# Kernel optimization log

Hardware: AMD Instinct MI355X
Metric: run time of the kernel (lower is better)

The kernel has to match this reference:

```python
import jax, jax.numpy as jnp
import numpy as np

NUM_HEADS = 16
HEAD_DIM = 64
DIM = NUM_HEADS * HEAD_DIM
ROPE_BASE = 10000.0
EPS = 1e-6


def rotate_half(x):
    # pairs (x0,x1) -> (-x1, x0), interleaved on last dim
    x_even = x[..., ::2]
    x_odd = x[..., 1::2]
    return jnp.stack((-x_odd, x_even), axis=-1).reshape(x.shape)


def apply_rope(q, k, positions, base=ROPE_BASE):
    d = q.shape[-1]
    inv_freq = 1.0 / (base ** (jnp.arange(0, d, 2, dtype=jnp.float32) / d))
    angles = positions.astype(jnp.float32)[..., None] * inv_freq  # [B, L, d/2]
    cos = jnp.repeat(jnp.cos(angles), 2, axis=-1).astype(q.dtype)[:, None, :, :]  # [B,1,L,d]
    sin = jnp.repeat(jnp.sin(angles), 2, axis=-1).astype(q.dtype)[:, None, :, :]
    return q * cos + rotate_half(q) * sin, k * cos + rotate_half(k) * sin


def per_head_layernorm(x, weight):
    # x: [B, H, L, d]; weight: [H, d]; bias is zeros (qkv_bias=False)
    mu = jnp.mean(x, axis=-1, keepdims=True)
    var = jnp.mean(jnp.square(x - mu), axis=-1, keepdims=True)
    xn = (x - mu) * jax.lax.rsqrt(var + EPS)
    return xn * weight[None, :, None, :]


def setup_inputs() -> dict:
    key = jax.random.key(0)
    k1, k2, k3, k4, k5 = jax.random.split(key, 5)
    B, L = 2, 2048
    x = jax.random.normal(k1, (B, L, DIM), dtype=jnp.float32)
    mask = jnp.ones((B, L, L), dtype=bool)
    positions = jnp.broadcast_to(jnp.arange(L, dtype=jnp.int64 if jax.config.jax_enable_x64 else jnp.int32), (B, L))
    s = 1.0 / np.sqrt(DIM)
    W_qkv = jax.random.normal(k2, (DIM, 3 * DIM), dtype=jnp.float32) * s
    W_out = jax.random.normal(k3, (DIM, DIM), dtype=jnp.float32) * s
    qn_w = jnp.ones((NUM_HEADS, HEAD_DIM), dtype=jnp.float32)
    kn_w = jnp.ones((NUM_HEADS, HEAD_DIM), dtype=jnp.float32)
    return {"x": x, "mask": mask, "positions": positions,
            "W_qkv": W_qkv, "W_out": W_out, "qn_w": qn_w, "kn_w": kn_w}


def reference(x, mask, positions, W_qkv, W_out, qn_w, kn_w):
    B, L, D = x.shape
    scale = HEAD_DIM ** -0.5
    qkv = x @ W_qkv  # [B, L, 3D]
    qkv = qkv.reshape(B, L, 3, NUM_HEADS, HEAD_DIM)
    qkv = jnp.transpose(qkv, (2, 0, 3, 1, 4))  # [3, B, H, L, d]
    q, k, v = qkv[0], qkv[1], qkv[2]
    q = per_head_layernorm(q, qn_w)
    k = per_head_layernorm(k, kn_w)
    q, k = apply_rope(q, k, positions)
    attn = jnp.einsum('bhqd,bhkd->bhqk', q, k) * scale  # [B, H, L, L]
    attn = jnp.where(mask[:, None, :, :], attn, -jnp.inf)
    attn = jax.nn.softmax(attn, axis=-1)
    out = jnp.einsum('bhqk,bhkd->bhqd', attn, v)  # [B, H, L, d]
    out = jnp.transpose(out, (0, 2, 1, 3)).reshape(B, L, D)
    return out @ W_out
```

## Files before the change

### kernel.cpp

```cpp
#include <hip/hip_runtime.h>


typedef __bf16 bf16x8 __attribute__((ext_vector_type(8)));
typedef __bf16 bf16x2 __attribute__((ext_vector_type(2)));
typedef float f32x4 __attribute__((ext_vector_type(4)));

#define QSCALE 0.1803368802f

__device__ __forceinline__ float bf2f(unsigned short u) {
  unsigned int v = ((unsigned int)u) << 16;
  float f;
  __builtin_memcpy(&f, &v, 4);
  return f;
}
__device__ __forceinline__ unsigned short f2bf(float f) {
  unsigned int v;
  __builtin_memcpy(&v, &f, 4);
  v += 0x7fffu + ((v >> 16) & 1u);
  return (unsigned short)(v >> 16);
}
__device__ __forceinline__ unsigned short f2bf_hw(float f) {
  __bf16 h = (__bf16)f;
  unsigned short u;
  __builtin_memcpy(&u, &h, 2);
  return u;
}
__device__ __forceinline__ unsigned int pack2(float a, float b) {
  bf16x2 t;
  t[0] = (__bf16)a;
  t[1] = (__bf16)b;
  unsigned int u;
  __builtin_memcpy(&u, &t, 4);
  return u;
}
__device__ __forceinline__ void gl_lds16(const unsigned short* g, unsigned short* l) {
  __builtin_amdgcn_global_load_lds(
      (const __attribute__((address_space(1))) unsigned int*)g,
      (__attribute__((address_space(3))) unsigned int*)l, 16, 0, 0);
}

__global__ __launch_bounds__(256) void prep(
    const float* __restrict__ x, const float* __restrict__ W_qkv,
    const float* __restrict__ W_out, const int* __restrict__ positions,
    unsigned short* __restrict__ xb,
    unsigned short* __restrict__ Wt_qkv, unsigned short* __restrict__ Wt_out,
    float2* __restrict__ lut) {
  __shared__ float tile[64][65];
  const int bid = blockIdx.x, t = threadIdx.x;
  if (bid < 4096) {
    int i = (bid * 256 + t) * 4;
    float4 v = *reinterpret_cast<const float4*>(x + i);
    ushort4 o;
    o.x = f2bf(v.x); o.y = f2bf(v.y); o.z = f2bf(v.z); o.w = f2bf(v.w);
    *reinterpret_cast<ushort4*>(xb + i) = o;
    return;
  }
  if (bid >= 5120) {
    int idx = (bid - 5120) * 256 + t;
    int m = idx >> 5, p = idx & 31;
    float pos = (float)positions[m];
    float invf = __builtin_amdgcn_exp2f(-(float)(2 * p) * (13.2877124f / 64.0f));
    float rev = pos * invf * 0.15915494f;
    rev -= floorf(rev);
    lut[idx] = make_float2(__builtin_amdgcn_cosf(rev), __builtin_amdgcn_sinf(rev));
    return;
  }
  const float* W; unsigned short* Wt; int Nd, bn, bk;
  if (bid < 4864) {
    int id = bid - 4096; W = W_qkv; Wt = Wt_qkv; Nd = 3072; bn = id % 48; bk = id / 48;
  } else {
    int id = bid - 4864; W = W_out; Wt = Wt_out; Nd = 1024; bn = id % 16; bk = id / 16;
  }
  const int Kd = 1024;
#pragma unroll
  for (int i = 0; i < 16; i++) {
    int idx = i * 256 + t;
    int k = idx >> 6, n = idx & 63;
    tile[k][n] = W[(size_t)(bk * 64 + k) * Nd + bn * 64 + n];
  }
  __syncthreads();
#pragma unroll
  for (int i = 0; i < 16; i++) {
    int idx = i * 256 + t;
    int n = idx >> 6, k = idx & 63;
    Wt[(size_t)(bn * 64 + n) * Kd + bk * 64 + k] = f2bf(tile[k][n]);
  }
}

__global__ __launch_bounds__(256, 3) void gemm_qkv(
    const unsigned short* __restrict__ A,
    const unsigned short* __restrict__ Bt,
    const float* __restrict__ qn_w, const float* __restrict__ kn_w,
    const float2* __restrict__ lut,
    unsigned short* __restrict__ Qr,
    unsigned short* __restrict__ Kr,
    unsigned short* __restrict__ Vt, int K) {
  __shared__ __align__(16) unsigned short As[2][128 * 32];
  __shared__ __align__(16) unsigned short Bs[2][128 * 32];
  const int tid = threadIdx.x;
  const int lane = tid & 63, wid = tid >> 6;
  const int quad = lane >> 4, l16 = lane & 15;
  const int wr = wid >> 1, wc = wid & 1;
  const int bn = blockIdx.x, bm = blockIdx.y;
  const unsigned short* Ab = A + (size_t)bm * 128 * K;
  const unsigned short* Bb = Bt + (size_t)bn * 128 * K;

  f32x4 acc[4][4] = {};

  const int c0 = tid, c1 = tid + 256;
  const int ar0 = c0 >> 2, ag0 = ((c0 & 3) ^ ((ar0 >> 1) & 3)) * 8;
  const int ar1 = c1 >> 2, ag1 = ((c1 & 3) ^ ((ar1 >> 1) & 3)) * 8;

  gl_lds16(Ab + (size_t)ar0 * K + ag0, &As[0][c0 * 8]);
  gl_lds16(Ab + (size_t)ar1 * K + ag1, &As[0][c1 * 8]);
  gl_lds16(Bb + (size_t)ar0 * K + ag0, &Bs[0][c0 * 8]);
  gl_lds16(Bb + (size_t)ar1 * K + ag1, &Bs[0][c1 * 8]);

  const int iters = K >> 5;
  for (int it = 0; it < iters; it++) {
    const int cur = it & 1;
    __builtin_amdgcn_s_barrier();
    if (it + 1 < iters) {
      const int k0 = (it + 1) << 5, nb = cur ^ 1;
      gl_lds16(Ab + (size_t)ar0 * K + k0 + ag0, &As[nb][c0 * 8]);
      gl_lds16(Ab + (size_t)ar1 * K + k0 + ag1, &As[nb][c1 * 8]);
      gl_lds16(Bb + (size_t)ar0 * K + k0 + ag0, &Bs[nb][c0 * 8]);
      gl_lds16(Bb + (size_t)ar1 * K + k0 + ag1, &Bs[nb][c1 * 8]);
      __builtin_amdgcn_sched_barrier(0);
      asm volatile("s_waitcnt vmcnt(4)" ::: "memory");
    } else {
      __builtin_amdgcn_sched_barrier(0);
      asm volatile("s_waitcnt vmcnt(0)" ::: "memory");
    }
    __builtin_amdgcn_sched_barrier(0);
    __builtin_amdgcn_s_setprio(1);
    const unsigned short* Ac = As[cur];
    const unsigned short* Bc = Bs[cur];
    bf16x8 af[4], bfr[4];
#pragma unroll
    for (int i = 0; i < 4; i++) {
      int m = wr * 64 + i * 16 + l16;
      af[i] = *reinterpret_cast<const bf16x8*>(&Ac[m * 32 + ((quad ^ ((m >> 1) & 3)) * 8)]);
    }
#pragma unroll
    for (int j = 0; j < 4; j++) {
      int n = wc * 64 + j * 16 + l16;
      bfr[j] = *reinterpret_cast<const bf16x8*>(&Bc[n * 32 + ((quad ^ ((n >> 1) & 3)) * 8)]);
    }
#pragma unroll
    for (int i = 0; i < 4; i++)
#pragma unroll
      for (int j = 0; j < 4; j++)
        acc[i][j] = __builtin_amdgcn_mfma_f32_16x16x32_bf16(af[i], bfr[j], acc[i][j], 0, 0, 0);
    __builtin_amdgcn_s_setprio(0);
  }

  const int sec = bn >> 3;
  const int h = (bn & 7) * 2 + wc;
  const int b = bm >> 4;
  if (sec < 2) {
    const float* gw = sec ? kn_w : qn_w;
    unsigned short* dst = sec ? Kr : Qr;
    const float oscale = sec ? 1.0f : QSCALE;
    float w4[4];
#pragma unroll
    for (int j = 0; j < 4; j++) w4[j] = gw[h * 64 + j * 16 + l16];
#pragma unroll
    for (int i = 0; i < 4; i++)
#pragma unroll
      for (int r = 0; r < 4; r++) {
        int m = bm * 128 + wr * 64 + i * 16 + quad * 4 + r;
        int l = m & 2047;
        const float2* lrow = lut + m * 32;
        float2 cs4[4];
#pragma unroll
        for (int j = 0; j < 4; j++) cs4[j] = lrow[j * 8 + (l16 >> 1)];
        float sum = acc[i][0][r] + acc[i][1][r] + acc[i][2][r] + acc[i][3][r];
        float sq = acc[i][0][r] * acc[i][0][r] + acc[i][1][r] * acc[i][1][r] +
                   acc[i][2][r] * acc[i][2][r] + acc[i][3][r] * acc[i][3][r];
#pragma unroll
        for (int off = 1; off < 16; off <<= 1) {
          sum += __shfl_xor(sum, off);
          sq += __shfl_xor(sq, off);
        }
        float mu = sum * (1.0f / 64.0f);
        float var = sq * (1.0f / 64.0f) - mu * mu;
        float rs = rsqrtf(fmaxf(var, 0.0f) + 1e-6f);
#pragma unroll
        for (int j = 0; j < 4; j++) {
          float y = (acc[i][j][r] - mu) * rs * w4[j];
          float p = __shfl_xor(y, 1);
          float o = (l16 & 1) ? (y * cs4[j].x + p * cs4[j].y)
                              : (y * cs4[j].x - p * cs4[j].y);
          dst[((size_t)(b * 16 + h) * 2048 + l) * 64 + j * 16 + l16] = f2bf(o * oscale);
        }
      }
  } else {
#pragma unroll
    for (int i = 0; i < 4; i++) {
      int lp = (bm * 128 + wr * 64 + (i >> 1) * 32 + quad * 8 + (i & 1) * 4) & 2047;
#pragma unroll
      for (int j = 0; j < 4; j++) {
        int d = j * 16 + l16;
        uint2 v;
        v.x = pack2(acc[i][j][0], acc[i][j][1]);
        v.y = pack2(acc[i][j][2], acc[i][j][3]);
        *reinterpret_cast<uint2*>(&Vt[((size_t)(b * 16 + h) * 64 + d) * 2048 + lp]) = v;
      }
    }
  }
}

__global__ __launch_bounds__(512, 4) void attn_kernel(
    const unsigned short* __restrict__ Q,
    const unsigned short* __restrict__ K,
    const unsigned short* __restrict__ Vt,
    unsigned short* __restrict__ O) {
  __shared__ __align__(16) unsigned short Ks[2][2][64 * 64];
  __shared__ __align__(16) unsigned short Vs[2][2][64 * 64];

  int bid = blockIdx.x;
  int id = (bid & 7) * 64 + (bid >> 3);
  const int qt = id & 15; id >>= 4;
  const int h = id & 15;  const int b = id >> 4;
  const int tid = threadIdx.x;
  const int lane = tid & 63, wid = tid >> 6;
  const int half = wid >> 2, wg = wid & 3;
  const int quad = lane >> 4, l16 = lane & 15;

  const unsigned short* Qb = Q + (size_t)(b * 16 + h) * 2048 * 64;
  const unsigned short* Kb = K + (size_t)(b * 16 + h) * 2048 * 64;
  const unsigned short* Vb = Vt + (size_t)(b * 16 + h) * 64 * 2048;

  const int qbase = qt * 128 + wg * 32;
  bf16x8 qf[2][2];
#pragma unroll
  for (int g = 0; g < 2; g++)
#pragma unroll
    for (int d = 0; d < 2; d++)
      qf[g][d] = *reinterpret_cast<const bf16x8*>(
          &Qb[(size_t)(qbase + g * 16 + l16) * 64 + d * 32 + quad * 8]);

  bf16x8 ones8;
#pragma unroll
  for (int i = 0; i < 8; i++) ones8[i] = (__bf16)1.0f;

  f32x4 o[2][4] = {};
  f32x4 lacc[2] = {};

  const int ltid = tid & 255;
  const int c0 = ltid, c1 = ltid + 256;
  const int r0 = c0 >> 3, g0 = ((c0 & 7) ^ (r0 & 7)) * 8;
  const int r1 = c1 >> 3, g1 = ((c1 & 7) ^ (r1 & 7)) * 8;
  const int kb0 = half * 1024;

  gl_lds16(&Kb[(size_t)(kb0 + r0) * 64 + g0], &Ks[half][0][c0 * 8]);
  gl_lds16(&Kb[(size_t)(kb0 + r1) * 64 + g1], &Ks[half][0][c1 * 8]);
  gl_lds16(&Vb[(size_t)r0 * 2048 + kb0 + g0], &Vs[half][0][c0 * 8]);
  gl_lds16(&Vb[(size_t)r1 * 2048 + kb0 + g1], &Vs[half][0][c1 * 8]);

  for (int kt = 0; kt < 16; kt++) {
    const int cur = kt & 1;
    __builtin_amdgcn_s_barrier();
    if (kt + 1 < 16) {
      const int ko = kb0 + (kt + 1) * 64, nb = cur ^ 1;
      gl_lds16(&Kb[(size_t)(ko + r0) * 64 + g0], &Ks[half][nb][c0 * 8]);
      gl_lds16(&Kb[(size_t)(ko + r1) * 64 + g1], &Ks[half][nb][c1 * 8]);
      gl_lds16(&Vb[(size_t)r0 * 2048 + ko + g0], &Vs[half][nb][c0 * 8]);
      gl_lds16(&Vb[(size_t)r1 * 2048 + ko + g1], &Vs[half][nb][c1 * 8]);
      __builtin_amdgcn_sched_barrier(0);
      asm volatile("s_waitcnt vmcnt(4)" ::: "memory");
    } else {
      __builtin_amdgcn_sched_barrier(0);
      asm volatile("s_waitcnt vmcnt(0)" ::: "memory");
    }
    __builtin_amdgcn_sched_barrier(0);
    const unsigned short* Kc = Ks[half][cur];
    const unsigned short* Vc = Vs[half][cur];

    __builtin_amdgcn_s_setprio(1);
    f32x4 s4a[4] = {}, s4b[4] = {};
#pragma unroll
    for (int kg = 0; kg < 4; kg++) {
      int row = kg * 16 + l16;
      bf16x8 kf0 = *reinterpret_cast<const bf16x8*>(
          &Kc[row * 64 + ((quad ^ (row & 7)) * 8)]);
      bf16x8 kf1 = *reinterpret_cast<const bf16x8*>(
          &Kc[row * 64 + (((4 + quad) ^ (row & 7)) * 8)]);
      s4a[kg] = __builtin_amdgcn_mfma_f32_16x16x32_bf16(kf0, qf[0][0], s4a[kg], 0, 0, 0);
      s4a[kg] = __builtin_amdgcn_mfma_f32_16x16x32_bf16(kf1, qf[0][1], s4a[kg], 0, 0, 0);
      s4b[kg] = __builtin_amdgcn_mfma_f32_16x16x32_bf16(kf0, qf[1][0], s4b[kg], 0, 0, 0);
      s4b[kg] = __builtin_amdgcn_mfma_f32_16x16x32_bf16(kf1, qf[1][1], s4b[kg], 0, 0, 0);
    }
    float pva[4][4], pvb[4][4];
#pragma unroll
    for (int kg = 0; kg < 4; kg++)
#pragma unroll
      for (int r = 0; r < 4; r++) {
        pva[kg][r] = __builtin_amdgcn_exp2f(s4a[kg][r]);
        pvb[kg][r] = __builtin_amdgcn_exp2f(s4b[kg][r]);
      }
    union u32x4v { unsigned int u[4]; bf16x8 v; };
    u32x4v paa[2], pab[2];
#pragma unroll
    for (int c = 0; c < 2; c++) {
      paa[c].u[0] = pack2(pva[c * 2][0], pva[c * 2][1]);
      paa[c].u[1] = pack2(pva[c * 2][2], pva[c * 2][3]);
      paa[c].u[2] = pack2(pva[c * 2 + 1][0], pva[c * 2 + 1][1]);
      paa[c].u[3] = pack2(pva[c * 2 + 1][2], pva[c * 2 + 1][3]);
      pab[c].u[0] = pack2(pvb[c * 2][0], pvb[c * 2][1]);
      pab[c].u[1] = pack2(pvb[c * 2][2], pvb[c * 2][3]);
      pab[c].u[2] = pack2(pvb[c * 2 + 1][0], pvb[c * 2 + 1][1]);
      pab[c].u[3] = pack2(pvb[c * 2 + 1][2], pvb[c * 2 + 1][3]);
    }
#pragma unroll
    for (int c = 0; c < 2; c++) {
      lacc[0] = __builtin_amdgcn_mfma_f32_16x16x32_bf16(paa[c].v, ones8, lacc[0], 0, 0, 0);
      lacc[1] = __builtin_amdgcn_mfma_f32_16x16x32_bf16(pab[c].v, ones8, lacc[1], 0, 0, 0);
#pragma unroll
      for (int i = 0; i < 4; i++) {
        int row = i * 16 + l16;
        bf16x8 vfr = *reinterpret_cast<const bf16x8*>(
            &Vc[row * 64 + (((c * 4 + quad) ^ (row & 7)) * 8)]);
        o[0][i] = __builtin_amdgcn_mfma_f32_16x16x32_bf16(paa[c].v, vfr, o[0][i], 0, 0, 0);
        o[1][i] = __builtin_amdgcn_mfma_f32_16x16x32_bf16(pab[c].v, vfr, o[1][i], 0, 0, 0);
      }
    }
    __builtin_amdgcn_s_setprio(0);
  }

  __syncthreads();
  float* Om = (float*)&Ks[0][0][0];
  float* Lm = (float*)&Vs[0][0][0];
  if (half == 0) {
#pragma unroll
    for (int g = 0; g < 2; g++) {
#pragma unroll
      for (int i = 0; i < 4; i++)
#pragma unroll
        for (int r = 0; r < 4; r++)
          Om[(wg * 32 + g * 16 + quad * 4 + r) * 64 + i * 16 + l16] = o[g][i][r];
      if (l16 == 0) {
#pragma unroll
        for (int r = 0; r < 4; r++)
          Lm[wg * 32 + g * 16 + quad * 4 + r] = lacc[g][r];
      }
    }
  }
  __syncthreads();
  if (half == 1) {
#pragma unroll
    for (int g = 0; g < 2; g++) {
#pragma unroll
      for (int r = 0; r < 4; r++) {
        float lt = lacc[g][r] + Lm[wg * 32 + g * 16 + quad * 4 + r];
        float inv = 1.0f / lt;
        int q = qbase + g * 16 + quad * 4 + r;
#pragma unroll
        for (int i = 0; i < 4; i++) {
          float sum = o[g][i][r] + Om[(wg * 32 + g * 16 + quad * 4 + r) * 64 + i * 16 + l16];
          O[((size_t)(b * 2048 + q)) * 1024 + h * 64 + i * 16 + l16] = f2bf_hw(sum * inv);
        }
      }
    }
  }
}

__global__ __launch_bounds__(256) void gemm_out(
    const unsigned short* __restrict__ A,
    const unsigned short* __restrict__ Bt,
    float* __restrict__ C, int M, int N, int K) {
  __shared__ __align__(16) unsigned short As[2][128 * 64];
  __shared__ __align__(16) unsigned short Bs[2][64 * 64];
  const int tid = threadIdx.x;
  const int lane = tid & 63, wid = tid >> 6;
  const int quad = lane >> 4, l16 = lane & 15;
  const int bn = blockIdx.x, bm = blockIdx.y;
  const unsigned short* Ab = A + (size_t)bm * 128 * K;
  const unsigned short* Bb = Bt + (size_t)bn * 64 * K;

  f32x4 acc[2][4] = {};

  int arow[4], asrc[4];
#pragma unroll
  for (int t2 = 0; t2 < 4; t2++) {
    int s = t2 * 256 + tid;
    arow[t2] = s >> 3;
    asrc[t2] = (((s & 7) ^ (arow[t2] & 7)) * 8);
  }
  int brow[2], bsrc[2];
#pragma unroll
  for (int t2 = 0; t2 < 2; t2++) {
    int s = t2 * 256 + tid;
    brow[t2] = s >> 3;
    bsrc[t2] = (((s & 7) ^ (brow[t2] & 7)) * 8);
  }

#pragma unroll
  for (int t2 = 0; t2 < 4; t2++)
    gl_lds16(Ab + (size_t)arow[t2] * K + asrc[t2], &As[0][(t2 * 256 + tid) * 8]);
#pragma unroll
  for (int t2 = 0; t2 < 2; t2++)
    gl_lds16(Bb + (size_t)brow[t2] * K + bsrc[t2], &Bs[0][(t2 * 256 + tid) * 8]);

  const int iters = K >> 6;
  for (int it = 0; it < iters; it++) {
    const int cur = it & 1;
    __builtin_amdgcn_s_barrier();
    if (it + 1 < iters) {
      const int k0 = (it + 1) << 6, nb = cur ^ 1;
#pragma unroll
      for (int t2 = 0; t2 < 4; t2++)
        gl_lds16(Ab + (size_t)arow[t2] * K + k0 + asrc[t2], &As[nb][(t2 * 256 + tid) * 8]);
#pragma unroll
      for (int t2 = 0; t2 < 2; t2++)
        gl_lds16(Bb + (size_t)brow[t2] * K + k0 + bsrc[t2], &Bs[nb][(t2 * 256 + tid) * 8]);
      __builtin_amdgcn_sched_barrier(0);
      asm volatile("s_waitcnt vmcnt(6)" ::: "memory");
    } else {
      __builtin_amdgcn_sched_barrier(0);
      asm volatile("s_waitcnt vmcnt(0)" ::: "memory");
    }
    __builtin_amdgcn_sched_barrier(0);
    __builtin_amdgcn_s_setprio(1);
    const unsigned short* Ac = As[cur];
    const unsigned short* Bc = Bs[cur];
    bf16x8 af[2][2], bfr[4][2];
#pragma unroll
    for (int i = 0; i < 2; i++) {
      int m = wid * 32 + i * 16 + l16;
#pragma unroll
      for (int kk = 0; kk < 2; kk++)
        af[i][kk] = *reinterpret_cast<const bf16x8*>(
            &Ac[(m * 8 + ((kk * 4 + quad) ^ (m & 7))) * 8]);
    }
#pragma unroll
    for (int j = 0; j < 4; j++) {
      int n = j * 16 + l16;
#pragma unroll
      for (int kk = 0; kk < 2; kk++)
        bfr[j][kk] = *reinterpret_cast<const bf16x8*>(
            &Bc[(n * 8 + ((kk * 4 + quad) ^ (n & 7))) * 8]);
    }
#pragma unroll
    for (int kk = 0; kk < 2; kk++)
#pragma unroll
      for (int i = 0; i < 2; i++)
#pragma unroll
        for (int j = 0; j < 4; j++)
          acc[i][j] = __builtin_amdgcn_mfma_f32_16x16x32_bf16(af[i][kk], bfr[j][kk], acc[i][j], 0, 0, 0);
    __builtin_amdgcn_s_setprio(0);
  }
#pragma unroll
  for (int i = 0; i < 2; i++)
#pragma unroll
    for (int j = 0; j < 4; j++)
#pragma unroll
      for (int r = 0; r < 4; r++) {
        int m = bm * 128 + wid * 32 + i * 16 + quad * 4 + r;
        int n = bn * 64 + j * 16 + l16;
        C[(size_t)m * N + n] = acc[i][j][r];
      }
}

extern "C" void kernel_launch(void* const* d_in, const int* in_sizes, int n_in,
                              void* d_out, int out_size, void* d_ws, size_t ws_size,
                              hipStream_t stream) {
  (void)in_sizes; (void)n_in; (void)out_size; (void)ws_size;
  const float* x     = (const float*)d_in[0];
  const int*   pos   = (const int*)d_in[2];
  const float* W_qkv = (const float*)d_in[3];
  const float* W_out = (const float*)d_in[4];
  const float* qn_w  = (const float*)d_in[5];
  const float* kn_w  = (const float*)d_in[6];
  float*       out   = (float*)d_out;

  char* ws = (char*)d_ws;
  unsigned short* xb     = (unsigned short*)(ws);
  unsigned short* Qr     = (unsigned short*)(ws + 8388608);
  unsigned short* Kr     = (unsigned short*)(ws + 16777216);
  unsigned short* Vt     = (unsigned short*)(ws + 25165824);
  unsigned short* Wt_qkv = (unsigned short*)(ws + 33554432);
  unsigned short* Wt_out = (unsigned short*)(ws + 39845888);
  float2*         lut    = (float2*)(ws + 41943040);
  unsigned short* attn_o = xb;

  prep<<<5632, 256, 0, stream>>>(x, W_qkv, W_out, pos, xb, Wt_qkv, Wt_out, lut);
  gemm_qkv<<<dim3(24, 32), 256, 0, stream>>>(xb, Wt_qkv, qn_w, kn_w, lut, Qr, Kr, Vt, 1024);
  attn_kernel<<<512, 512, 0, stream>>>(Qr, Kr, Vt, attn_o);
  gemm_out<<<dim3(16, 32), 256, 0, stream>>>(attn_o, Wt_out, out, 4096, 1024, 1024);
}
```

Baseline: 199.1 us.

## Fuse Q/K/V column tiles per head pair into one block sharing A tile

Each block now computes the Q, K and V outputs for one 128-row slab and one head pair, loading the activation tile once and three weight tiles into LDS. The grid shrinks to 256 blocks of 512 threads, and each wave handles 32 rows across three sections. This removes the repeated loading of the same activation rows by three separate blocks. In exchange, LDS per block and register pressure rise, and with only one block per CU, latency hiding may drop.

```diff
diff --git a/kernel.cpp b/kernel.cpp
--- a/kernel.cpp
+++ b/kernel.cpp
@@ -87,7 +87,7 @@
   }
 }
 
-__global__ __launch_bounds__(256, 3) void gemm_qkv(
+__global__ __launch_bounds__(512, 2) void gemm_qkv(
     const unsigned short* __restrict__ A,
     const unsigned short* __restrict__ Bt,
     const float* __restrict__ qn_w, const float* __restrict__ kn_w,
@@ -96,25 +96,27 @@
     unsigned short* __restrict__ Kr,
     unsigned short* __restrict__ Vt, int K) {
   __shared__ __align__(16) unsigned short As[2][128 * 32];
-  __shared__ __align__(16) unsigned short Bs[2][128 * 32];
+  __shared__ __align__(16) unsigned short Bs[2][3 * 128 * 32];
   const int tid = threadIdx.x;
   const int lane = tid & 63, wid = tid >> 6;
   const int quad = lane >> 4, l16 = lane & 15;
   const int wr = wid >> 1, wc = wid & 1;
-  const int bn = blockIdx.x, bm = blockIdx.y;
+  const int bid = blockIdx.x;
+  const int hp = bid & 7;
+  const int bm = bid >> 3;
   const unsigned short* Ab = A + (size_t)bm * 128 * K;
-  const unsigned short* Bb = Bt + (size_t)bn * 128 * K;
-
-  f32x4 acc[4][4] = {};
-
-  const int c0 = tid, c1 = tid + 256;
-  const int ar0 = c0 >> 2, ag0 = ((c0 & 3) ^ ((ar0 >> 1) & 3)) * 8;
-  const int ar1 = c1 >> 2, ag1 = ((c1 & 3) ^ ((ar1 >> 1) & 3)) * 8;
-
-  gl_lds16(Ab + (size_t)ar0 * K + ag0, &As[0][c0 * 8]);
-  gl_lds16(Ab + (size_t)ar1 * K + ag1, &As[0][c1 * 8]);
-  gl_lds16(Bb + (size_t)ar0 * K + ag0, &Bs[0][c0 * 8]);
-  gl_lds16(Bb + (size_t)ar1 * K + ag1, &Bs[0][c1 * 8]);
+  const unsigned short* Bq = Bt + (size_t)(hp * 128) * K;
+  const unsigned short* Bk = Bt + (size_t)(1024 + hp * 128) * K;
+  const unsigned short* Bv = Bt + (size_t)(2048 + hp * 128) * K;
+
+  f32x4 acc[3][2][4] = {};
+
+  const int srow = tid >> 2, sgrp = ((tid & 3) ^ ((srow >> 1) & 3)) * 8;
+
+  gl_lds16(Ab + (size_t)srow * K + sgrp, &As[0][tid * 8]);
+  gl_lds16(Bq + (size_t)srow * K + sgrp, &Bs[0][tid * 8]);
+  gl_lds16(Bk + (size_t)srow * K + sgrp, &Bs[0][(512 + tid) * 8]);
+  gl_lds16(Bv + (size_t)srow * K + sgrp, &Bs[0][(1024 + tid) * 8]);
 
   const int iters = K >> 5;
   for (int it = 0; it < iters; it++) {
@@ -122,10 +124,10 @@
     __builtin_amdgcn_s_barrier();
     if (it + 1 < iters) {
       const int k0 = (it + 1) << 5, nb = cur ^ 1;
-      gl_lds16(Ab + (size_t)ar0 * K + k0 + ag0, &As[nb][c0 * 8]);
-      gl_lds16(Ab + (size_t)ar1 * K + k0 + ag1, &As[nb][c1 * 8]);
-      gl_lds16(Bb + (size_t)ar0 * K + k0 + ag0, &Bs[nb][c0 * 8]);
-      gl_lds16(Bb + (size_t)ar1 * K + k0 + ag1, &Bs[nb][c1 * 8]);
+      gl_lds16(Ab + (size_t)srow * K + k0 + sgrp, &As[nb][tid * 8]);
+      gl_lds16(Bq + (size_t)srow * K + k0 + sgrp, &Bs[nb][tid * 8]);
+      gl_lds16(Bk + (size_t)srow * K + k0 + sgrp, &Bs[nb][(512 + tid) * 8]);
+      gl_lds16(Bv + (size_t)srow * K + k0 + sgrp, &Bs[nb][(1024 + tid) * 8]);
       __builtin_amdgcn_sched_barrier(0);
       asm volatile("s_waitcnt vmcnt(4)" ::: "memory");
     } else {
@@ -136,29 +138,36 @@
     __builtin_amdgcn_s_setprio(1);
     const unsigned short* Ac = As[cur];
     const unsigned short* Bc = Bs[cur];
-    bf16x8 af[4], bfr[4];
-#pragma unroll
-    for (int i = 0; i < 4; i++) {
-      int m = wr * 64 + i * 16 + l16;
+    bf16x8 af[2];
+#pragma unroll
+    for (int i = 0; i < 2; i++) {
+      int m = wr * 32 + i * 16 + l16;
       af[i] = *reinterpret_cast<const bf16x8*>(&Ac[m * 32 + ((quad ^ ((m >> 1) & 3)) * 8)]);
     }
 #pragma unroll
-    for (int j = 0; j < 4; j++) {
-      int n = wc * 64 + j * 16 + l16;
-      bfr[j] = *reinterpret_cast<const bf16x8*>(&Bc[n * 32 + ((quad ^ ((n >> 1) & 3)) * 8)]);
-    }
-#pragma unroll
-    for (int i = 0; i < 4; i++)
-#pragma unroll
-      for (int j = 0; j < 4; j++)
-        acc[i][j] = __builtin_amdgcn_mfma_f32_16x16x32_bf16(af[i], bfr[j], acc[i][j], 0, 0, 0);
+    for (int sec = 0; sec < 3; sec++) {
+      bf16x8 bfr[4];
+#pragma unroll
+      for (int j = 0; j < 4; j++) {
+        int n = wc * 64 + j * 16 + l16;
+        bfr[j] = *reinterpret_cast<const bf16x8*>(
+            &Bs[cur][sec * 4096 + n * 32 + ((quad ^ ((n >> 1) & 3)) * 8)]);
+      }
+#pragma unroll
+      for (int i = 0; i < 2; i++)
+#pragma unroll
+        for (int j = 0; j < 4; j++)
+          acc[sec][i][j] = __builtin_amdgcn_mfma_f32_16x16x32_bf16(af[i], bfr[j], acc[sec][i][j], 0, 0, 0);
+    }
     __builtin_amdgcn_s_setprio(0);
-  }
-
-  const int sec = bn >> 3;
-  const int h = (bn & 7) * 2 + wc;
+    (void)Bc;
+  }
+
+  const int h = hp * 2 + wc;
   const int b = bm >> 4;
-  if (sec < 2) {
+
+#pragma unroll
+  for (int sec = 0; sec < 2; sec++) {
     const float* gw = sec ? kn_w : qn_w;
     unsigned short* dst = sec ? Kr : Qr;
     const float oscale = sec ? 1.0f : QSCALE;
@@ -166,18 +175,18 @@
 #pragma unroll
     for (int j = 0; j < 4; j++) w4[j] = gw[h * 64 + j * 16 + l16];
 #pragma unroll
-    for (int i = 0; i < 4; i++)
+    for (int i = 0; i < 2; i++)
 #pragma unroll
       for (int r = 0; r < 4; r++) {
-        int m = bm * 128 + wr * 64 + i * 16 + quad * 4 + r;
+        int m = bm * 128 + wr * 32 + i * 16 + quad * 4 + r;
         int l = m & 2047;
         const float2* lrow = lut + m * 32;
         float2 cs4[4];
 #pragma unroll
         for (int j = 0; j < 4; j++) cs4[j] = lrow[j * 8 + (l16 >> 1)];
-        float sum = acc[i][0][r] + acc[i][1][r] + acc[i][2][r] + acc[i][3][r];
-        float sq = acc[i][0][r] * acc[i][0][r] + acc[i][1][r] * acc[i][1][r] +
-                   acc[i][2][r] * acc[i][2][r] + acc[i][3][r] * acc[i][3][r];
+        float sum = acc[sec][i][0][r] + acc[sec][i][1][r] + acc[sec][i][2][r] + acc[sec][i][3][r];
+        float sq = acc[sec][i][0][r] * acc[sec][i][0][r] + acc[sec][i][1][r] * acc[sec][i][1][r] +
+                   acc[sec][i][2][r] * acc[sec][i][2][r] + acc[sec][i][3][r] * acc[sec][i][3][r];
 #pragma unroll
         for (int off = 1; off < 16; off <<= 1) {
           sum += __shfl_xor(sum, off);
@@ -188,25 +197,24 @@
         float rs = rsqrtf(fmaxf(var, 0.0f) + 1e-6f);
 #pragma unroll
         for (int j = 0; j < 4; j++) {
-          float y = (acc[i][j][r] - mu) * rs * w4[j];
+          float y = (acc[sec][i][j][r] - mu) * rs * w4[j];
           float p = __shfl_xor(y, 1);
           float o = (l16 & 1) ? (y * cs4[j].x + p * cs4[j].y)
                               : (y * cs4[j].x - p * cs4[j].y);
           dst[((size_t)(b * 16 + h) * 2048 + l) * 64 + j * 16 + l16] = f2bf(o * oscale);
         }
       }
-  } else {
-#pragma unroll
-    for (int i = 0; i < 4; i++) {
-      int lp = (bm * 128 + wr * 64 + (i >> 1) * 32 + quad * 8 + (i & 1) * 4) & 2047;
-#pragma unroll
-      for (int j = 0; j < 4; j++) {
-        int d = j * 16 + l16;
-        uint2 v;
-        v.x = pack2(acc[i][j][0], acc[i][j][1]);
-        v.y = pack2(acc[i][j][2], acc[i][j][3]);
-        *reinterpret_cast<uint2*>(&Vt[((size_t)(b * 16 + h) * 64 + d) * 2048 + lp]) = v;
-      }
+  }
+#pragma unroll
+  for (int i = 0; i < 2; i++) {
+    int lp = (bm * 128 + wr * 32 + quad * 8 + i * 4) & 2047;
+#pragma unroll
+    for (int j = 0; j < 4; j++) {
+      int d = j * 16 + l16;
+      uint2 v;
+      v.x = pack2(acc[2][i][j][0], acc[2][i][j][1]);
+      v.y = pack2(acc[2][i][j][2], acc[2][i][j][3]);
+      *reinterpret_cast<uint2*>(&Vt[((size_t)(b * 16 + h) * 64 + d) * 2048 + lp]) = v;
     }
   }
 }
@@ -486,7 +494,7 @@
   unsigned short* attn_o = xb;
 
   prep<<<5632, 256, 0, stream>>>(x, W_qkv, W_out, pos, xb, Wt_qkv, Wt_out, lut);
-  gemm_qkv<<<dim3(24, 32), 256, 0, stream>>>(xb, Wt_qkv, qn_w, kn_w, lut, Qr, Kr, Vt, 1024);
+  gemm_qkv<<<256, 512, 0, stream>>>(xb, Wt_qkv, qn_w, kn_w, lut, Qr, Kr, Vt, 1024);
   attn_kernel<<<512, 512, 0, stream>>>(Qr, Kr, Vt, attn_o);
   gemm_out<<<dim3(16, 32), 256, 0, stream>>>(attn_o, Wt_out, out, 4096, 1024, 1024);
 }
```

Measured after the change: 203.6 us. 2.2% more time.
